# Performance work log

Measured on AMD Instinct MI355X. Metric: run time of the kernel, lower is better.

## Reference

```python
import jax, jax.numpy as jnp
import numpy as np

B, S, D, H = 2, 2048, 1024, 16
HD = D // H  # head_dim = 64


def setup_inputs() -> dict:
    key = jax.random.key(0)
    ks = jax.random.split(key, 8)
    std = 1.0 / np.sqrt(D)
    return {
        "q": jax.random.normal(ks[0], (B, S, D), jnp.float32),
        "k": jax.random.normal(ks[1], (B, S, D), jnp.float32),
        "v": jax.random.normal(ks[2], (B, S, D), jnp.float32),
        "attn_mask": jnp.ones((B, S, S), jnp.int32),
        "Wq": jax.random.normal(ks[3], (D, D), jnp.float32) * std,
        "bq": jnp.zeros((D,), jnp.float32),
        "Wk": jax.random.normal(ks[4], (D, D), jnp.float32) * std,
        "bk": jnp.zeros((D,), jnp.float32),
        "Wv": jax.random.normal(ks[5], (D, D), jnp.float32) * std,
        "bv": jnp.zeros((D,), jnp.float32),
        "Wo": jax.random.normal(ks[6], (D, D), jnp.float32) * std,
        "bo": jnp.zeros((D,), jnp.float32),
    }


def reference(q, k, v, attn_mask, Wq, bq, Wk, bk, Wv, bv, Wo, bo):
    # Linear projections (torch Linear: x @ W.T + b; here W stored as [in, out])
    Q = q @ Wq + bq
    K = k @ Wk + bk
    V = v @ Wv + bv
    # split heads: [B, H, S, HD]
    def split(x):
        return x.reshape(B, S, H, HD).transpose(0, 2, 1, 3)
    q_s, k_s, v_s = split(Q), split(K), split(V)
    # NOTE: original code calls scores.masked_fill(...) NON-in-place and
    # discards the result, so attn_mask has NO effect on the math.
    scale = 1.0 / np.sqrt(HD).astype(np.float32)
    scores = jnp.einsum("bhqd,bhkd->bhqk", q_s, k_s) * scale  # [B,H,S,S]
    attn = jax.nn.softmax(scores, axis=-1)
    context = jnp.einsum("bhqk,bhkd->bhqd", attn, v_s)
    context = context.transpose(0, 2, 1, 3).reshape(B, S, D)
    out = context @ Wo + bo
    return (out, attn)
```

## Files before the change

kernel.cpp:

```cpp
#include <hip/hip_runtime.h>
#include <hip/hip_bf16.h>
#include <type_traits>

typedef __bf16 bf16;
typedef bf16 v8bf __attribute__((ext_vector_type(8)));
typedef float v4f __attribute__((ext_vector_type(4)));

constexpr int Bc = 2, Sc = 2048, Dc = 1024, Hc = 16, HDc = 64;
constexpr int Mr = Bc * Sc;

__device__ inline v4f mfma16(v8bf a, v8bf b, v4f c) {
    return __builtin_amdgcn_mfma_f32_16x16x32_bf16(a, b, c, 0, 0, 0);
}

__global__ void wtrans_kernel(const float* __restrict__ Wq, const float* __restrict__ Wk,
                              const float* __restrict__ Wv, const float* __restrict__ Wo,
                              bf16* __restrict__ out) {
    __shared__ float t[32][33];
    const float* W = (blockIdx.z == 0) ? Wq : (blockIdx.z == 1) ? Wk : (blockIdx.z == 2) ? Wv : Wo;
    bf16* Wt = out + (size_t)blockIdx.z * (Dc * Dc);
    int x0 = blockIdx.x * 32, y0 = blockIdx.y * 32;
    int tx = threadIdx.x, ty = threadIdx.y;
#pragma unroll
    for (int i = 0; i < 4; i++)
        t[ty + 8 * i][tx] = W[(size_t)(y0 + ty + 8 * i) * Dc + x0 + tx];
    __syncthreads();
#pragma unroll
    for (int i = 0; i < 4; i++)
        Wt[(size_t)(x0 + ty + 8 * i) * Dc + y0 + tx] = (bf16)t[tx][ty + 8 * i];
}

__global__ void vtrans_kernel(const bf16* __restrict__ V, bf16* __restrict__ Vt) {
    __shared__ bf16 t[32][33];
    int b = blockIdx.z;
    const bf16* Vb = V + (size_t)b * Sc * Dc;
    bf16* Vtb = Vt + (size_t)b * Dc * Sc;
    int s0 = blockIdx.x * 32, d0 = blockIdx.y * 32;
    int tx = threadIdx.x, ty = threadIdx.y;
#pragma unroll
    for (int i = 0; i < 4; i++)
        t[ty + 8 * i][tx] = Vb[(size_t)(s0 + ty + 8 * i) * Dc + d0 + tx];
    __syncthreads();
#pragma unroll
    for (int i = 0; i < 4; i++)
        Vtb[(size_t)(d0 + ty + 8 * i) * Sc + s0 + tx] = t[tx][ty + 8 * i];
}

template <typename TIn, typename TOut>
__global__ __launch_bounds__(256) void gemm_kernel(const TIn* __restrict__ X,
                                                   const bf16* __restrict__ Wt,
                                                   const float* __restrict__ bias,
                                                   TOut* __restrict__ Y) {
    constexpr int BK = 32;
    __shared__ bf16 As[128][BK + 8];
    __shared__ bf16 Bs[64][BK + 8];
    const int mTile = blockIdx.x * 128, nTile = blockIdx.y * 64;
    const int tid = threadIdx.x;
    const int w = tid >> 6, l = tid & 63, lr = l & 15, quad = l >> 4;
    const int wm = w & 1, wn = w >> 1;

    v4f acc[4][2];
#pragma unroll
    for (int mt = 0; mt < 4; mt++)
#pragma unroll
        for (int nt = 0; nt < 2; nt++) acc[mt][nt] = v4f{0.f, 0.f, 0.f, 0.f};

    const int arow = tid >> 1, acol0 = (tid & 1) * 16;
    const int brow = tid >> 2, bcol0 = (tid & 3) * 8;

    for (int kt = 0; kt < Dc; kt += BK) {
        __syncthreads();
        if constexpr (std::is_same_v<TIn, float>) {
            const float* src = X + (size_t)(mTile + arow) * Dc + kt + acol0;
            float4 f0 = *(const float4*)(src);
            float4 f1 = *(const float4*)(src + 4);
            float4 f2 = *(const float4*)(src + 8);
            float4 f3 = *(const float4*)(src + 12);
            v8bf v0, v1;
            v0[0] = (bf16)f0.x; v0[1] = (bf16)f0.y; v0[2] = (bf16)f0.z; v0[3] = (bf16)f0.w;
            v0[4] = (bf16)f1.x; v0[5] = (bf16)f1.y; v0[6] = (bf16)f1.z; v0[7] = (bf16)f1.w;
            v1[0] = (bf16)f2.x; v1[1] = (bf16)f2.y; v1[2] = (bf16)f2.z; v1[3] = (bf16)f2.w;
            v1[4] = (bf16)f3.x; v1[5] = (bf16)f3.y; v1[6] = (bf16)f3.z; v1[7] = (bf16)f3.w;
            *(v8bf*)&As[arow][acol0] = v0;
            *(v8bf*)&As[arow][acol0 + 8] = v1;
        } else {
            const v8bf* src = (const v8bf*)(X + (size_t)(mTile + arow) * Dc + kt + acol0);
            *(v8bf*)&As[arow][acol0] = src[0];
            *(v8bf*)&As[arow][acol0 + 8] = src[1];
        }
        *(v8bf*)&Bs[brow][bcol0] =
            *(const v8bf*)(Wt + (size_t)(nTile + brow) * Dc + kt + bcol0);
        __syncthreads();

        v8bf a[4], bf[2];
#pragma unroll
        for (int mt = 0; mt < 4; mt++)
            a[mt] = *(const v8bf*)&As[wm * 64 + mt * 16 + lr][quad * 8];
#pragma unroll
        for (int nt = 0; nt < 2; nt++)
            bf[nt] = *(const v8bf*)&Bs[wn * 32 + nt * 16 + lr][quad * 8];
#pragma unroll
        for (int mt = 0; mt < 4; mt++)
#pragma unroll
            for (int nt = 0; nt < 2; nt++)
                acc[mt][nt] = mfma16(a[mt], bf[nt], acc[mt][nt]);
    }

#pragma unroll
    for (int mt = 0; mt < 4; mt++)
#pragma unroll
        for (int nt = 0; nt < 2; nt++)
#pragma unroll
            for (int r = 0; r < 4; r++) {
                int row = mTile + wm * 64 + mt * 16 + quad * 4 + r;
                int col = nTile + wn * 32 + nt * 16 + lr;
                float vv = acc[mt][nt][r] + bias[col];
                Y[(size_t)row * Dc + col] = (TOut)vv;
            }
}

__global__ __launch_bounds__(256) void attn_kernel(const bf16* __restrict__ Q,
                                                   const bf16* __restrict__ K,
                                                   const bf16* __restrict__ Vt,
                                                   float* __restrict__ attn,
                                                   bf16* __restrict__ ctx) {
    __shared__ bf16 Ps[4][16][40];
    const int b = blockIdx.z, h = blockIdx.y, rb = blockIdx.x;
    const int tid = threadIdx.x, w = tid >> 6, l = tid & 63, lr = l & 15, quad = l >> 4;
    const int r0 = rb * 64 + w * 16;
    const float scale = 0.125f;

    const bf16* Qrow = Q + (size_t)(b * Sc + r0 + lr) * Dc + h * HDc;
    v8bf qa0 = *(const v8bf*)(Qrow + quad * 8);
    v8bf qa1 = *(const v8bf*)(Qrow + 32 + quad * 8);

    const bf16* Kbase = K + (size_t)(b * Sc) * Dc + h * HDc;

    float sum[4] = {0.f, 0.f, 0.f, 0.f};
    for (int ct = 0; ct < Sc / 16; ct++) {
        const bf16* Krow = Kbase + (size_t)(ct * 16 + lr) * Dc;
        v8bf kb0 = *(const v8bf*)(Krow + quad * 8);
        v8bf kb1 = *(const v8bf*)(Krow + 32 + quad * 8);
        v4f s = v4f{0.f, 0.f, 0.f, 0.f};
        s = mfma16(qa0, kb0, s);
        s = mfma16(qa1, kb1, s);
#pragma unroll
        for (int r = 0; r < 4; r++) sum[r] += __expf(s[r] * scale);
    }
#pragma unroll
    for (int r = 0; r < 4; r++) {
#pragma unroll
        for (int off = 1; off < 16; off <<= 1) sum[r] += __shfl_xor(sum[r], off, 16);
    }
    float inv[4];
#pragma unroll
    for (int r = 0; r < 4; r++) inv[r] = 1.0f / sum[r];

    float* attnBase = attn + ((size_t)((b * Hc + h) * Sc + r0)) * Sc;
    const bf16* VtBase = Vt + (size_t)(b * Dc + h * HDc) * Sc;
    v4f acc[4];
#pragma unroll
    for (int nt = 0; nt < 4; nt++) acc[nt] = v4f{0.f, 0.f, 0.f, 0.f};

    for (int ctp = 0; ctp < Sc / 32; ctp++) {
#pragma unroll
        for (int half = 0; half < 2; half++) {
            int ct = ctp * 2 + half;
            const bf16* Krow = Kbase + (size_t)(ct * 16 + lr) * Dc;
            v8bf kb0 = *(const v8bf*)(Krow + quad * 8);
            v8bf kb1 = *(const v8bf*)(Krow + 32 + quad * 8);
            v4f s = v4f{0.f, 0.f, 0.f, 0.f};
            s = mfma16(qa0, kb0, s);
            s = mfma16(qa1, kb1, s);
#pragma unroll
            for (int r = 0; r < 4; r++) {
                float p = __expf(s[r] * scale) * inv[r];
                attnBase[(size_t)(quad * 4 + r) * Sc + ct * 16 + lr] = p;
                Ps[w][quad * 4 + r][half * 16 + lr] = (bf16)p;
            }
        }
        __syncthreads();
        v8bf pa = *(const v8bf*)&Ps[w][lr][quad * 8];
#pragma unroll
        for (int nt = 0; nt < 4; nt++) {
            v8bf vb = *(const v8bf*)(VtBase + (size_t)(nt * 16 + lr) * Sc + ctp * 32 + quad * 8);
            acc[nt] = mfma16(pa, vb, acc[nt]);
        }
    }

#pragma unroll
    for (int nt = 0; nt < 4; nt++)
#pragma unroll
        for (int r = 0; r < 4; r++) {
            size_t row = (size_t)(b * Sc + r0 + quad * 4 + r);
            ctx[row * Dc + h * HDc + nt * 16 + lr] = (bf16)acc[nt][r];
        }
}

extern "C" void kernel_launch(void* const* d_in, const int* in_sizes, int n_in,
                              void* d_out, int out_size, void* d_ws, size_t ws_size,
                              hipStream_t stream) {
    const float* q  = (const float*)d_in[0];
    const float* k  = (const float*)d_in[1];
    const float* v  = (const float*)d_in[2];
    const float* Wq = (const float*)d_in[4];
    const float* bq = (const float*)d_in[5];
    const float* Wk = (const float*)d_in[6];
    const float* bk = (const float*)d_in[7];
    const float* Wv = (const float*)d_in[8];
    const float* bv = (const float*)d_in[9];
    const float* Wo = (const float*)d_in[10];
    const float* bo = (const float*)d_in[11];

    char* ws = (char*)d_ws;
    bf16* Qbf = (bf16*)(ws);
    bf16* Kbf = (bf16*)(ws + 8388608);
    bf16* Vbf = (bf16*)(ws + 16777216);
    bf16* Vt  = (bf16*)(ws + 25165824);
    bf16* ctx = (bf16*)(ws + 33554432);
    bf16* Wts = (bf16*)(ws + 41943040);
    bf16* Wqt = Wts;
    bf16* Wkt = Wts + 1 * (size_t)(Dc * Dc);
    bf16* Wvt = Wts + 2 * (size_t)(Dc * Dc);
    bf16* Wot = Wts + 3 * (size_t)(Dc * Dc);

    float* outp = (float*)d_out;
    float* attn = outp + (size_t)Mr * Dc;

    wtrans_kernel<<<dim3(32, 32, 4), dim3(32, 8), 0, stream>>>(Wq, Wk, Wv, Wo, Wts);
    gemm_kernel<float, bf16><<<dim3(32, 16), 256, 0, stream>>>(q, Wqt, bq, Qbf);
    gemm_kernel<float, bf16><<<dim3(32, 16), 256, 0, stream>>>(k, Wkt, bk, Kbf);
    gemm_kernel<float, bf16><<<dim3(32, 16), 256, 0, stream>>>(v, Wvt, bv, Vbf);
    vtrans_kernel<<<dim3(64, 32, 2), dim3(32, 8), 0, stream>>>(Vbf, Vt);
    attn_kernel<<<dim3(32, 16, 2), 256, 0, stream>>>(Qbf, Kbf, Vt, attn, ctx);
    gemm_kernel<bf16, float><<<dim3(32, 16), 256, 0, stream>>>(ctx, Wot, bo, outp);
}
```

Measured before the change: 1.063 ms.

## Pre-convert inputs to bf16, use direct-to-LDS GEMM loads, pipeline attention loop

Adds a separate fp32-to-bf16 conversion kernel so the GEMM reads bf16 only. The GEMM now loads its tiles with global_load_lds directly into LDS, uses BK=64 and keeps the bias in registers. The attention kernel computes S^T via swapped MFMA operands so each lane owns one row, which leaves a single cross-lane reduction. It also prefetches the next K/V tiles, writes attn rows with vectorised nontemporal stores, and swaps the block barrier for an lgkmcnt wait. In exchange there are extra conversion passes and the unpadded LDS tiles may cause bank conflicts.

```diff
diff --git a/kernel.cpp b/kernel.cpp
--- a/kernel.cpp
+++ b/kernel.cpp
@@ -1,9 +1,9 @@
 #include <hip/hip_runtime.h>
 #include <hip/hip_bf16.h>
-#include <type_traits>
 
 typedef __bf16 bf16;
 typedef bf16 v8bf __attribute__((ext_vector_type(8)));
+typedef bf16 v4bf __attribute__((ext_vector_type(4)));
 typedef float v4f __attribute__((ext_vector_type(4)));
 
 constexpr int Bc = 2, Sc = 2048, Dc = 1024, Hc = 16, HDc = 64;
@@ -11,6 +11,11 @@
 
 __device__ inline v4f mfma16(v8bf a, v8bf b, v4f c) {
     return __builtin_amdgcn_mfma_f32_16x16x32_bf16(a, b, c, 0, 0, 0);
+}
+
+__device__ inline void gload_lds16(const void* g, void* l) {
+    __builtin_amdgcn_global_load_lds((__attribute__((address_space(1))) void*)g,
+                                     (__attribute__((address_space(3))) void*)l, 16, 0, 0);
 }
 
 __global__ void wtrans_kernel(const float* __restrict__ Wq, const float* __restrict__ Wk,
@@ -30,6 +35,16 @@
         Wt[(size_t)(x0 + ty + 8 * i) * Dc + y0 + tx] = (bf16)t[tx][ty + 8 * i];
 }
 
+__global__ void cvt_kernel(const float* __restrict__ in, bf16* __restrict__ out) {
+    size_t i = ((size_t)blockIdx.x * blockDim.x + threadIdx.x) * 8;
+    float4 f0 = *(const float4*)(in + i);
+    float4 f1 = *(const float4*)(in + i + 4);
+    v8bf v;
+    v[0] = (bf16)f0.x; v[1] = (bf16)f0.y; v[2] = (bf16)f0.z; v[3] = (bf16)f0.w;
+    v[4] = (bf16)f1.x; v[5] = (bf16)f1.y; v[6] = (bf16)f1.z; v[7] = (bf16)f1.w;
+    *(v8bf*)(out + i) = v;
+}
+
 __global__ void vtrans_kernel(const bf16* __restrict__ V, bf16* __restrict__ Vt) {
     __shared__ bf16 t[32][33];
     int b = blockIdx.z;
@@ -46,18 +61,18 @@
         Vtb[(size_t)(d0 + ty + 8 * i) * Sc + s0 + tx] = t[tx][ty + 8 * i];
 }
 
-template <typename TIn, typename TOut>
-__global__ __launch_bounds__(256) void gemm_kernel(const TIn* __restrict__ X,
+template <typename TOut>
+__global__ __launch_bounds__(256) void gemm_kernel(const bf16* __restrict__ X,
                                                    const bf16* __restrict__ Wt,
                                                    const float* __restrict__ bias,
                                                    TOut* __restrict__ Y) {
-    constexpr int BK = 32;
-    __shared__ bf16 As[128][BK + 8];
-    __shared__ bf16 Bs[64][BK + 8];
+    __shared__ bf16 As[128][64];
+    __shared__ bf16 Bs[64][64];
     const int mTile = blockIdx.x * 128, nTile = blockIdx.y * 64;
     const int tid = threadIdx.x;
     const int w = tid >> 6, l = tid & 63, lr = l & 15, quad = l >> 4;
     const int wm = w & 1, wn = w >> 1;
+    const int srow = l >> 3, scol = (l & 7) * 8;
 
     v4f acc[4][2];
 #pragma unroll
@@ -65,45 +80,45 @@
 #pragma unroll
         for (int nt = 0; nt < 2; nt++) acc[mt][nt] = v4f{0.f, 0.f, 0.f, 0.f};
 
-    const int arow = tid >> 1, acol0 = (tid & 1) * 16;
-    const int brow = tid >> 2, bcol0 = (tid & 3) * 8;
-
-    for (int kt = 0; kt < Dc; kt += BK) {
+    float bv[2];
+#pragma unroll
+    for (int nt = 0; nt < 2; nt++) bv[nt] = bias[nTile + wn * 32 + nt * 16 + lr];
+
+    const bf16* Xbase = X + (size_t)mTile * Dc;
+    const bf16* Wbase = Wt + (size_t)nTile * Dc;
+
+    for (int kt = 0; kt < Dc; kt += 64) {
         __syncthreads();
-        if constexpr (std::is_same_v<TIn, float>) {
-            const float* src = X + (size_t)(mTile + arow) * Dc + kt + acol0;
-            float4 f0 = *(const float4*)(src);
-            float4 f1 = *(const float4*)(src + 4);
-            float4 f2 = *(const float4*)(src + 8);
-            float4 f3 = *(const float4*)(src + 12);
-            v8bf v0, v1;
-            v0[0] = (bf16)f0.x; v0[1] = (bf16)f0.y; v0[2] = (bf16)f0.z; v0[3] = (bf16)f0.w;
-            v0[4] = (bf16)f1.x; v0[5] = (bf16)f1.y; v0[6] = (bf16)f1.z; v0[7] = (bf16)f1.w;
-            v1[0] = (bf16)f2.x; v1[1] = (bf16)f2.y; v1[2] = (bf16)f2.z; v1[3] = (bf16)f2.w;
-            v1[4] = (bf16)f3.x; v1[5] = (bf16)f3.y; v1[6] = (bf16)f3.z; v1[7] = (bf16)f3.w;
-            *(v8bf*)&As[arow][acol0] = v0;
-            *(v8bf*)&As[arow][acol0 + 8] = v1;
-        } else {
-            const v8bf* src = (const v8bf*)(X + (size_t)(mTile + arow) * Dc + kt + acol0);
-            *(v8bf*)&As[arow][acol0] = src[0];
-            *(v8bf*)&As[arow][acol0 + 8] = src[1];
-        }
-        *(v8bf*)&Bs[brow][bcol0] =
-            *(const v8bf*)(Wt + (size_t)(nTile + brow) * Dc + kt + bcol0);
+#pragma unroll
+        for (int i = 0; i < 4; i++) {
+            int r = w * 32 + i * 8 + srow;
+            gload_lds16(Xbase + (size_t)r * Dc + kt + scol, &As[w * 32 + i * 8][0]);
+        }
+#pragma unroll
+        for (int i = 0; i < 2; i++) {
+            int r = w * 16 + i * 8 + srow;
+            gload_lds16(Wbase + (size_t)r * Dc + kt + scol, &Bs[w * 16 + i * 8][0]);
+        }
         __syncthreads();
 
-        v8bf a[4], bf[2];
+        v8bf a[4][2], bb[2][2];
 #pragma unroll
         for (int mt = 0; mt < 4; mt++)
-            a[mt] = *(const v8bf*)&As[wm * 64 + mt * 16 + lr][quad * 8];
+#pragma unroll
+            for (int kk = 0; kk < 2; kk++)
+                a[mt][kk] = *(const v8bf*)&As[wm * 64 + mt * 16 + lr][kk * 32 + quad * 8];
 #pragma unroll
         for (int nt = 0; nt < 2; nt++)
-            bf[nt] = *(const v8bf*)&Bs[wn * 32 + nt * 16 + lr][quad * 8];
-#pragma unroll
-        for (int mt = 0; mt < 4; mt++)
-#pragma unroll
-            for (int nt = 0; nt < 2; nt++)
-                acc[mt][nt] = mfma16(a[mt], bf[nt], acc[mt][nt]);
+#pragma unroll
+            for (int kk = 0; kk < 2; kk++)
+                bb[nt][kk] = *(const v8bf*)&Bs[wn * 32 + nt * 16 + lr][kk * 32 + quad * 8];
+#pragma unroll
+        for (int kk = 0; kk < 2; kk++)
+#pragma unroll
+            for (int mt = 0; mt < 4; mt++)
+#pragma unroll
+                for (int nt = 0; nt < 2; nt++)
+                    acc[mt][nt] = mfma16(a[mt][kk], bb[nt][kk], acc[mt][nt]);
     }
 
 #pragma unroll
@@ -114,8 +129,7 @@
             for (int r = 0; r < 4; r++) {
                 int row = mTile + wm * 64 + mt * 16 + quad * 4 + r;
                 int col = nTile + wn * 32 + nt * 16 + lr;
-                float vv = acc[mt][nt][r] + bias[col];
-                Y[(size_t)row * Dc + col] = (TOut)vv;
+                Y[(size_t)row * Dc + col] = (TOut)(acc[mt][nt][r] + bv[nt]);
             }
 }
 
@@ -136,56 +150,94 @@
 
     const bf16* Kbase = K + (size_t)(b * Sc) * Dc + h * HDc;
 
-    float sum[4] = {0.f, 0.f, 0.f, 0.f};
-    for (int ct = 0; ct < Sc / 16; ct++) {
-        const bf16* Krow = Kbase + (size_t)(ct * 16 + lr) * Dc;
-        v8bf kb0 = *(const v8bf*)(Krow + quad * 8);
-        v8bf kb1 = *(const v8bf*)(Krow + 32 + quad * 8);
-        v4f s = v4f{0.f, 0.f, 0.f, 0.f};
-        s = mfma16(qa0, kb0, s);
-        s = mfma16(qa1, kb1, s);
-#pragma unroll
-        for (int r = 0; r < 4; r++) sum[r] += __expf(s[r] * scale);
-    }
-#pragma unroll
-    for (int r = 0; r < 4; r++) {
-#pragma unroll
-        for (int off = 1; off < 16; off <<= 1) sum[r] += __shfl_xor(sum[r], off, 16);
-    }
-    float inv[4];
-#pragma unroll
-    for (int r = 0; r < 4; r++) inv[r] = 1.0f / sum[r];
-
-    float* attnBase = attn + ((size_t)((b * Hc + h) * Sc + r0)) * Sc;
+    float sum = 0.f, sumB = 0.f;
+    for (int ct = 0; ct < Sc / 16; ct += 2) {
+        const bf16* Kr0 = Kbase + (size_t)(ct * 16 + lr) * Dc;
+        const bf16* Kr1 = Kr0 + 16 * Dc;
+        v8bf k00 = *(const v8bf*)(Kr0 + quad * 8);
+        v8bf k01 = *(const v8bf*)(Kr0 + 32 + quad * 8);
+        v8bf k10 = *(const v8bf*)(Kr1 + quad * 8);
+        v8bf k11 = *(const v8bf*)(Kr1 + 32 + quad * 8);
+        v4f s0 = v4f{0.f, 0.f, 0.f, 0.f}, s1 = v4f{0.f, 0.f, 0.f, 0.f};
+        s0 = mfma16(k00, qa0, s0);
+        s0 = mfma16(k01, qa1, s0);
+        s1 = mfma16(k10, qa0, s1);
+        s1 = mfma16(k11, qa1, s1);
+#pragma unroll
+        for (int r = 0; r < 4; r++) sum += __expf(s0[r] * scale);
+#pragma unroll
+        for (int r = 0; r < 4; r++) sumB += __expf(s1[r] * scale);
+    }
+    sum += sumB;
+    sum += __shfl_xor(sum, 16);
+    sum += __shfl_xor(sum, 32);
+    const float inv = 1.0f / sum;
+
+    float* attnRow = attn + ((size_t)((b * Hc + h) * Sc + r0 + lr)) * Sc;
     const bf16* VtBase = Vt + (size_t)(b * Dc + h * HDc) * Sc;
+
     v4f acc[4];
 #pragma unroll
     for (int nt = 0; nt < 4; nt++) acc[nt] = v4f{0.f, 0.f, 0.f, 0.f};
 
-    for (int ctp = 0; ctp < Sc / 32; ctp++) {
-#pragma unroll
-        for (int half = 0; half < 2; half++) {
-            int ct = ctp * 2 + half;
-            const bf16* Krow = Kbase + (size_t)(ct * 16 + lr) * Dc;
-            v8bf kb0 = *(const v8bf*)(Krow + quad * 8);
-            v8bf kb1 = *(const v8bf*)(Krow + 32 + quad * 8);
-            v4f s = v4f{0.f, 0.f, 0.f, 0.f};
-            s = mfma16(qa0, kb0, s);
-            s = mfma16(qa1, kb1, s);
-#pragma unroll
-            for (int r = 0; r < 4; r++) {
-                float p = __expf(s[r] * scale) * inv[r];
-                attnBase[(size_t)(quad * 4 + r) * Sc + ct * 16 + lr] = p;
-                Ps[w][quad * 4 + r][half * 16 + lr] = (bf16)p;
-            }
-        }
-        __syncthreads();
+    constexpr int NT = Sc / 32;
+    v8bf k00, k01, k10, k11, vb[4];
+    {
+        const bf16* Kr0 = Kbase + (size_t)lr * Dc;
+        const bf16* Kr1 = Kr0 + 16 * Dc;
+        k00 = *(const v8bf*)(Kr0 + quad * 8);
+        k01 = *(const v8bf*)(Kr0 + 32 + quad * 8);
+        k10 = *(const v8bf*)(Kr1 + quad * 8);
+        k11 = *(const v8bf*)(Kr1 + 32 + quad * 8);
+#pragma unroll
+        for (int nt = 0; nt < 4; nt++)
+            vb[nt] = *(const v8bf*)(VtBase + (size_t)(nt * 16 + lr) * Sc + quad * 8);
+    }
+
+    for (int ctp = 0; ctp < NT; ctp++) {
+        v4f s0 = v4f{0.f, 0.f, 0.f, 0.f}, s1 = v4f{0.f, 0.f, 0.f, 0.f};
+        s0 = mfma16(k00, qa0, s0);
+        s0 = mfma16(k01, qa1, s0);
+        s1 = mfma16(k10, qa0, s1);
+        s1 = mfma16(k11, qa1, s1);
+
+        const int nc = (ctp + 1 < NT) ? ctp + 1 : ctp;
+        const bf16* Kr0n = Kbase + (size_t)(nc * 32 + lr) * Dc;
+        const bf16* Kr1n = Kr0n + 16 * Dc;
+        v8bf n00 = *(const v8bf*)(Kr0n + quad * 8);
+        v8bf n01 = *(const v8bf*)(Kr0n + 32 + quad * 8);
+        v8bf n10 = *(const v8bf*)(Kr1n + quad * 8);
+        v8bf n11 = *(const v8bf*)(Kr1n + 32 + quad * 8);
+        v8bf vn[4];
+#pragma unroll
+        for (int nt = 0; nt < 4; nt++)
+            vn[nt] = *(const v8bf*)(VtBase + (size_t)(nt * 16 + lr) * Sc + nc * 32 + quad * 8);
+
+        v4f p0, p1;
+        v4bf pb0, pb1;
+#pragma unroll
+        for (int r = 0; r < 4; r++) {
+            p0[r] = __expf(s0[r] * scale) * inv;
+            pb0[r] = (bf16)p0[r];
+        }
+#pragma unroll
+        for (int r = 0; r < 4; r++) {
+            p1[r] = __expf(s1[r] * scale) * inv;
+            pb1[r] = (bf16)p1[r];
+        }
+        __builtin_nontemporal_store(p0, (v4f*)(attnRow + ctp * 32 + quad * 4));
+        __builtin_nontemporal_store(p1, (v4f*)(attnRow + ctp * 32 + 16 + quad * 4));
+        *(v4bf*)&Ps[w][lr][quad * 4] = pb0;
+        *(v4bf*)&Ps[w][lr][16 + quad * 4] = pb1;
+        asm volatile("s_waitcnt lgkmcnt(0)" ::: "memory");
+        __builtin_amdgcn_sched_barrier(0);
         v8bf pa = *(const v8bf*)&Ps[w][lr][quad * 8];
 #pragma unroll
-        for (int nt = 0; nt < 4; nt++) {
-            v8bf vb = *(const v8bf*)(VtBase + (size_t)(nt * 16 + lr) * Sc + ctp * 32 + quad * 8);
-            acc[nt] = mfma16(pa, vb, acc[nt]);
-        }
+        for (int nt = 0; nt < 4; nt++) acc[nt] = mfma16(pa, vb[nt], acc[nt]);
+
+        k00 = n00; k01 = n01; k10 = n10; k11 = n11;
+#pragma unroll
+        for (int nt = 0; nt < 4; nt++) vb[nt] = vn[nt];
     }
 
 #pragma unroll
@@ -213,25 +265,32 @@
     const float* bo = (const float*)d_in[11];
 
     char* ws = (char*)d_ws;
-    bf16* Qbf = (bf16*)(ws);
-    bf16* Kbf = (bf16*)(ws + 8388608);
-    bf16* Vbf = (bf16*)(ws + 16777216);
-    bf16* Vt  = (bf16*)(ws + 25165824);
-    bf16* ctx = (bf16*)(ws + 33554432);
-    bf16* Wts = (bf16*)(ws + 41943040);
+    const size_t MB8 = 8388608;
+    bf16* T0  = (bf16*)(ws);
+    bf16* Qbf = (bf16*)(ws + 1 * MB8);
+    bf16* Kbf = (bf16*)(ws + 2 * MB8);
+    bf16* Vbf = (bf16*)(ws + 3 * MB8);
+    bf16* Vt  = (bf16*)(ws + 4 * MB8);
+    bf16* Wts = (bf16*)(ws + 5 * MB8);
     bf16* Wqt = Wts;
     bf16* Wkt = Wts + 1 * (size_t)(Dc * Dc);
     bf16* Wvt = Wts + 2 * (size_t)(Dc * Dc);
     bf16* Wot = Wts + 3 * (size_t)(Dc * Dc);
+    bf16* ctx = Vbf;
 
     float* outp = (float*)d_out;
     float* attn = outp + (size_t)Mr * Dc;
 
     wtrans_kernel<<<dim3(32, 32, 4), dim3(32, 8), 0, stream>>>(Wq, Wk, Wv, Wo, Wts);
-    gemm_kernel<float, bf16><<<dim3(32, 16), 256, 0, stream>>>(q, Wqt, bq, Qbf);
-    gemm_kernel<float, bf16><<<dim3(32, 16), 256, 0, stream>>>(k, Wkt, bk, Kbf);
-    gemm_kernel<float, bf16><<<dim3(32, 16), 256, 0, stream>>>(v, Wvt, bv, Vbf);
+
+    cvt_kernel<<<dim3(2048), 256, 0, stream>>>(q, T0);
+    gemm_kernel<bf16><<<dim3(32, 16), 256, 0, stream>>>(T0, Wqt, bq, Qbf);
+    cvt_kernel<<<dim3(2048), 256, 0, stream>>>(k, T0);
+    gemm_kernel<bf16><<<dim3(32, 16), 256, 0, stream>>>(T0, Wkt, bk, Kbf);
+    cvt_kernel<<<dim3(2048), 256, 0, stream>>>(v, T0);
+    gemm_kernel<bf16><<<dim3(32, 16), 256, 0, stream>>>(T0, Wvt, bv, Vbf);
+
     vtrans_kernel<<<dim3(64, 32, 2), dim3(32, 8), 0, stream>>>(Vbf, Vt);
     attn_kernel<<<dim3(32, 16, 2), 256, 0, stream>>>(Qbf, Kbf, Vt, attn, ctx);
-    gemm_kernel<bf16, float><<<dim3(32, 16), 256, 0, stream>>>(ctx, Wot, bo, outp);
-}
+    gemm_kernel<float><<<dim3(32, 16), 256, 0, stream>>>(ctx, Wot, bo, outp);
+}
```

After: 972.6 us. -8.5%, faster.
